# Performance work log

Measured on AMD Instinct MI355X. Metric: run time of the kernel, lower is better.

The kernel has to match this reference:

```python
import jax, jax.numpy as jnp
import numpy as np

B, S, D, H, F = 4, 2048, 1024, 16, 4096
HD = D // H
EPS = 1e-6
ROPE_BASE = 10000.0


def apply_rope(x, positions, head_dim):
    # x: [B, S, H, hd], positions: [B, S]
    fraction = 2.0 * jnp.arange(0, head_dim // 2, dtype=jnp.float32) / head_dim
    timescale = ROPE_BASE ** fraction                      # [hd/2]
    angle = positions[:, :, None, None].astype(jnp.float32) / timescale  # [B,S,1,hd/2]
    sin, cos = jnp.sin(angle), jnp.cos(angle)
    first, second = jnp.split(x, 2, axis=-1)
    return jnp.concatenate([first * cos - second * sin,
                            second * cos + first * sin], axis=-1).astype(x.dtype)


def rms_norm(x, scale):
    var = jnp.mean(jnp.square(x), axis=-1, keepdims=True)
    return (x * jax.lax.rsqrt(var + EPS)) * scale


def setup_inputs() -> dict:
    key = jax.random.key(0)
    ks = jax.random.split(key, 10)
    std = 0.02
    x = jax.random.normal(ks[0], (B, S, D), dtype=jnp.float32)
    segment_positions = jnp.broadcast_to(jnp.arange(S, dtype=jnp.int32), (B, S))
    mask = jnp.broadcast_to(jnp.tril(jnp.ones((S, S), dtype=bool))[None, None], (B, 1, S, S))
    wq = jax.random.normal(ks[1], (D, H, HD), dtype=jnp.float32) * std
    wk = jax.random.normal(ks[2], (D, H, HD), dtype=jnp.float32) * std
    wv = jax.random.normal(ks[3], (D, H, HD), dtype=jnp.float32) * std
    wo = jax.random.normal(ks[4], (H, HD, D), dtype=jnp.float32) * std
    w_gate = jax.random.normal(ks[5], (D, F), dtype=jnp.float32) * std
    w_up = jax.random.normal(ks[6], (D, F), dtype=jnp.float32) * std
    w_down = jax.random.normal(ks[7], (F, D), dtype=jnp.float32) * std
    norm1 = jnp.ones((D,), dtype=jnp.float32)
    norm2 = jnp.ones((D,), dtype=jnp.float32)
    return dict(x=x, segment_positions=segment_positions, mask=mask,
                wq=wq, wk=wk, wv=wv, wo=wo,
                w_gate=w_gate, w_up=w_up, w_down=w_down,
                norm1=norm1, norm2=norm2)


def reference(x, segment_positions, mask, wq, wk, wv, wo, w_gate, w_up, w_down, norm1, norm2):
    # --- pre-norm RoPE attention residual block ---
    h = rms_norm(x, norm1)                                  # [B,S,D]
    q = jnp.einsum('bsd,dhk->bshk', h, wq)                  # [B,S,H,hd]
    k = jnp.einsum('bsd,dhk->bshk', h, wk)
    v = jnp.einsum('bsd,dhk->bshk', h, wv)
    q = apply_rope(q, segment_positions, HD)
    k = apply_rope(k, segment_positions, HD)
    q = q / jnp.sqrt(jnp.float32(HD))
    attn = jnp.einsum('bqhd,bkhd->bhqk', q, k)              # [B,H,S,S]
    big_neg = jnp.finfo(jnp.float32).min
    attn = jnp.where(mask, attn, big_neg)
    attn = jax.nn.softmax(attn, axis=-1)
    ctx = jnp.einsum('bhqk,bkhd->bqhd', attn, v)            # [B,S,H,hd]
    x = x + jnp.einsum('bqhd,hdo->bqo', ctx, wo)            # residual
    # --- pre-norm GLU FFN residual block ---
    h = rms_norm(x, norm2)
    gated = jax.nn.gelu(h @ w_gate) * (h @ w_up)            # [B,S,F]
    x = x + gated @ w_down
    return x
```

## Files before the change

kernel.cpp:

```cpp
#include <hip/hip_runtime.h>
#include <cstdint>
#include <cstddef>

#define BQ 4
#define SQ 2048
#define DQ 1024
#define HQ 16
#define HDQ 64
#define FQ 4096
#define MROWS (BQ * SQ)

typedef __attribute__((ext_vector_type(8))) __bf16 bf16x8;
typedef __attribute__((ext_vector_type(8))) short s16x8;
typedef __attribute__((ext_vector_type(4))) float f32x4;

__device__ __forceinline__ unsigned short f2bf(float f) {
  unsigned int u = __builtin_bit_cast(unsigned int, f);
  u = (u + 0x7FFFu + ((u >> 16) & 1u)) >> 16;
  return (unsigned short)u;
}
__device__ __forceinline__ float bf2f(unsigned short h) {
  unsigned int u = ((unsigned int)h) << 16;
  return __builtin_bit_cast(float, u);
}

typedef const unsigned int __attribute__((address_space(1))) *as1_cu32;
typedef unsigned int __attribute__((address_space(3))) *as3_u32;
#define GLD16(g, l) __builtin_amdgcn_global_load_lds((as1_cu32)(const void*)(g), (as3_u32)(void*)(l), 16, 0, 0)

__global__ __launch_bounds__(256) void k_transpose_bf16(const float* __restrict__ src,
                                                        unsigned short* __restrict__ dst,
                                                        int R, int C) {
  __shared__ float tile[32][33];
  int tx = threadIdx.x & 31, ty = threadIdx.x >> 5;
  int c0 = blockIdx.x * 32, r0 = blockIdx.y * 32;
#pragma unroll
  for (int i = 0; i < 32; i += 8)
    tile[ty + i][tx] = src[(size_t)(r0 + ty + i) * C + (c0 + tx)];
  __syncthreads();
#pragma unroll
  for (int i = 0; i < 32; i += 8)
    dst[(size_t)(c0 + ty + i) * R + (r0 + tx)] = f2bf(tile[tx][ty + i]);
}

__global__ __launch_bounds__(256) void k_rmsnorm(const float* __restrict__ x,
                                                 const float* __restrict__ g,
                                                 unsigned short* __restrict__ out) {
  int row = blockIdx.x, tid = threadIdx.x;
  const float4 v = ((const float4*)(x + (size_t)row * DQ))[tid];
  float ss = v.x * v.x + v.y * v.y + v.z * v.z + v.w * v.w;
#pragma unroll
  for (int d = 32; d >= 1; d >>= 1) ss += __shfl_xor(ss, d);
  __shared__ float ws4[4];
  if ((tid & 63) == 0) ws4[tid >> 6] = ss;
  __syncthreads();
  float tot = ws4[0] + ws4[1] + ws4[2] + ws4[3];
  float r = rsqrtf(tot * (1.0f / DQ) + 1e-6f);
  const float4 gv = ((const float4*)g)[tid];
  ushort4 o;
  o.x = f2bf(v.x * r * gv.x);
  o.y = f2bf(v.y * r * gv.y);
  o.z = f2bf(v.z * r * gv.z);
  o.w = f2bf(v.w * r * gv.w);
  ((ushort4*)(out + (size_t)row * DQ))[tid] = o;
}

template <int MODE>
__global__ __launch_bounds__(256) void k_gemm_bt(const unsigned short* __restrict__ A,
                                                 const unsigned short* __restrict__ Bt,
                                                 void* __restrict__ Cp,
                                                 const float* __restrict__ Res,
                                                 int M, int N, int K) {
  __shared__ __align__(16) unsigned short As[128 * 32];
  __shared__ __align__(16) unsigned short Bs[128 * 32];
  const int tid = threadIdx.x;
  const int lane = tid & 63, w = tid >> 6;
  const int m0 = blockIdx.y * 128, n0 = blockIdx.x * 128;
  const int wm = (w >> 1) * 64, wn = (w & 1) * 64;
  const int lr = lane & 15, lg = lane >> 4;
  f32x4 acc[4][4] = {};
  for (int k0 = 0; k0 < K; k0 += 32) {
#pragma unroll
    for (int i = 0; i < 2; ++i) {
      int flat = i * 256 + tid;
      int row = flat >> 2, ch = flat & 3;
      GLD16(A + (size_t)(m0 + row) * K + k0 + ch * 8, As + (size_t)(i * 256 + w * 64) * 8);
      GLD16(Bt + (size_t)(n0 + row) * K + k0 + ch * 8, Bs + (size_t)(i * 256 + w * 64) * 8);
    }
    __syncthreads();
    bf16x8 af[4], bfr[4];
#pragma unroll
    for (int mi = 0; mi < 4; ++mi)
      af[mi] = *(const bf16x8*)(As + (wm + mi * 16 + lr) * 32 + lg * 8);
#pragma unroll
    for (int ni = 0; ni < 4; ++ni)
      bfr[ni] = *(const bf16x8*)(Bs + (wn + ni * 16 + lr) * 32 + lg * 8);
#pragma unroll
    for (int mi = 0; mi < 4; ++mi)
#pragma unroll
      for (int ni = 0; ni < 4; ++ni)
        acc[mi][ni] = __builtin_amdgcn_mfma_f32_16x16x32_bf16(af[mi], bfr[ni], acc[mi][ni], 0, 0, 0);
    __syncthreads();
  }
#pragma unroll
  for (int mi = 0; mi < 4; ++mi) {
#pragma unroll
    for (int r = 0; r < 4; ++r) {
      int gr = m0 + wm + mi * 16 + lg * 4 + r;
#pragma unroll
      for (int ni = 0; ni < 4; ++ni) {
        int gc = n0 + wn + ni * 16 + lr;
        size_t idx = (size_t)gr * N + gc;
        float v = acc[mi][ni][r];
        if (MODE == 0) {
          ((unsigned short*)Cp)[idx] = f2bf(v);
        } else if (MODE == 1) {
          ((float*)Cp)[idx] = v + Res[idx];
        } else {
          float u = bf2f(((unsigned short*)Cp)[idx]);
          float t = v + 0.044715f * v * v * v;
          float gl = 0.5f * v * (1.0f + tanhf(0.7978845608028654f * t));
          ((unsigned short*)Cp)[idx] = f2bf(gl * u);
        }
      }
    }
  }
}

__global__ __launch_bounds__(512) void k_rope(const unsigned short* __restrict__ qkv,
                                              const int* __restrict__ pos,
                                              unsigned short* __restrict__ qp,
                                              unsigned short* __restrict__ kp,
                                              unsigned short* __restrict__ vp) {
  int bs = blockIdx.x;
  int b = bs >> 11, s = bs & 2047;
  int t = threadIdx.x;
  int hh = t >> 5, j = t & 31;
  float fp = (float)pos[bs];
  const unsigned short* row = qkv + (size_t)bs * 3072;
  float q1 = bf2f(row[hh * 64 + j]);
  float q2 = bf2f(row[hh * 64 + 32 + j]);
  float k1 = bf2f(row[1024 + hh * 64 + j]);
  float k2 = bf2f(row[1024 + hh * 64 + 32 + j]);
  float ts = powf(10000.0f, (float)j * (1.0f / 32.0f));
  float ang = fp / ts;
  float sn = sinf(ang), cs = cosf(ang);
  size_t o = ((size_t)(b * HQ + hh) * SQ + s) * HDQ + j;
  qp[o]      = f2bf((q1 * cs - q2 * sn) * 0.125f);
  qp[o + 32] = f2bf((q2 * cs + q1 * sn) * 0.125f);
  kp[o]      = f2bf(k1 * cs - k2 * sn);
  kp[o + 32] = f2bf(k2 * cs + k1 * sn);
  vp[o]      = row[2048 + hh * 64 + j];
  vp[o + 32] = row[2048 + hh * 64 + 32 + j];
}

__global__ __launch_bounds__(256) void k_flash(const unsigned short* __restrict__ qp,
                                               const unsigned short* __restrict__ kp,
                                               const unsigned short* __restrict__ vp,
                                               unsigned short* __restrict__ ctx) {
  int qb = (int)gridDim.x - 1 - (int)blockIdx.x;
  int bh = blockIdx.y;
  int b = bh >> 4, hh = bh & 15;
  __shared__ __align__(16) unsigned short Ks[32 * 64];
  __shared__ __align__(16) unsigned short Vt[64 * 40];
  __shared__ __align__(16) unsigned short Ps[4][16 * 32];
  int tid = threadIdx.x, lane = tid & 63, w = tid >> 6;
  const int lr = lane & 15, lg = lane >> 4;
  size_t hoff = (size_t)bh * SQ * HDQ;
  const unsigned short* Q = qp + hoff;
  const unsigned short* Kg = kp + hoff;
  const unsigned short* Vg = vp + hoff;
  int qr0 = qb * 64 + w * 16;
  bf16x8 aq0 = *(const bf16x8*)(Q + (size_t)(qr0 + lr) * 64 + lg * 8);
  bf16x8 aq1 = *(const bf16x8*)(Q + (size_t)(qr0 + lr) * 64 + 32 + lg * 8);
  f32x4 accO[4] = {};
  float mrow[4] = {-1e30f, -1e30f, -1e30f, -1e30f};
  float lrow[4] = {0.f, 0.f, 0.f, 0.f};
  int nt = qb * 2 + 2;
  for (int t = 0; t < nt; ++t) {
    int kv0 = t * 32;
    {
      int krow = tid >> 3, ch = tid & 7;
      GLD16(Kg + (size_t)(kv0 + krow) * 64 + ch * 8, Ks + (size_t)(w * 64) * 8);
    }
    {
      int rr = tid & 31, cb = (tid >> 5) * 8;
      bf16x8 vv = *(const bf16x8*)(Vg + (size_t)(kv0 + rr) * 64 + cb);
      s16x8 vs = __builtin_bit_cast(s16x8, vv);
#pragma unroll
      for (int jj = 0; jj < 8; ++jj)
        Vt[(cb + jj) * 40 + rr] = (unsigned short)vs[jj];
    }
    __syncthreads();
    f32x4 sacc[2] = {};
#pragma unroll
    for (int nh = 0; nh < 2; ++nh) {
      bf16x8 bk0 = *(const bf16x8*)(Ks + (nh * 16 + lr) * 64 + lg * 8);
      bf16x8 bk1 = *(const bf16x8*)(Ks + (nh * 16 + lr) * 64 + 32 + lg * 8);
      sacc[nh] = __builtin_amdgcn_mfma_f32_16x16x32_bf16(aq0, bk0, sacc[nh], 0, 0, 0);
      sacc[nh] = __builtin_amdgcn_mfma_f32_16x16x32_bf16(aq1, bk1, sacc[nh], 0, 0, 0);
    }
    float scl[4];
#pragma unroll
    for (int i = 0; i < 4; ++i) {
      int gr = qr0 + lg * 4 + i;
      float s0 = sacc[0][i], s1 = sacc[1][i];
      if (kv0 + lr > gr) s0 = -1e30f;
      if (kv0 + 16 + lr > gr) s1 = -1e30f;
      float mt = fmaxf(s0, s1);
#pragma unroll
      for (int dd = 8; dd >= 1; dd >>= 1) mt = fmaxf(mt, __shfl_xor(mt, dd));
      float mnew = fmaxf(mrow[i], mt);
      scl[i] = __expf(mrow[i] - mnew);
      float p0 = __expf(s0 - mnew), p1 = __expf(s1 - mnew);
      float ps = p0 + p1;
#pragma unroll
      for (int dd = 8; dd >= 1; dd >>= 1) ps += __shfl_xor(ps, dd);
      lrow[i] = lrow[i] * scl[i] + ps;
      mrow[i] = mnew;
      int prow = lg * 4 + i;
      Ps[w][prow * 32 + lr] = f2bf(p0);
      Ps[w][prow * 32 + 16 + lr] = f2bf(p1);
    }
#pragma unroll
    for (int n2 = 0; n2 < 4; ++n2) {
#pragma unroll
      for (int i = 0; i < 4; ++i) accO[n2][i] *= scl[i];
    }
    bf16x8 ap = *(const bf16x8*)(&Ps[w][lr * 32 + lg * 8]);
#pragma unroll
    for (int n2 = 0; n2 < 4; ++n2) {
      bf16x8 bv = *(const bf16x8*)(Vt + (n2 * 16 + lr) * 40 + lg * 8);
      accO[n2] = __builtin_amdgcn_mfma_f32_16x16x32_bf16(ap, bv, accO[n2], 0, 0, 0);
    }
    __syncthreads();
  }
  float linv[4];
#pragma unroll
  for (int i = 0; i < 4; ++i) linv[i] = 1.0f / lrow[i];
#pragma unroll
  for (int n2 = 0; n2 < 4; ++n2) {
#pragma unroll
    for (int i = 0; i < 4; ++i) {
      int gs = qr0 + lg * 4 + i;
      int gc = n2 * 16 + lr;
      ctx[((size_t)b * SQ + gs) * DQ + hh * 64 + gc] = f2bf(accO[n2][i] * linv[i]);
    }
  }
}

extern "C" void kernel_launch(void* const* d_in, const int* in_sizes, int n_in,
                              void* d_out, int out_size, void* d_ws, size_t ws_size,
                              hipStream_t stream) {
  (void)in_sizes; (void)n_in; (void)out_size; (void)ws_size;
  const float* x   = (const float*)d_in[0];
  const int*   pos = (const int*)d_in[1];
  const float* wq  = (const float*)d_in[3];
  const float* wk  = (const float*)d_in[4];
  const float* wv  = (const float*)d_in[5];
  const float* wo  = (const float*)d_in[6];
  const float* wg  = (const float*)d_in[7];
  const float* wu  = (const float*)d_in[8];
  const float* wd  = (const float*)d_in[9];
  const float* n1  = (const float*)d_in[10];
  const float* n2v = (const float*)d_in[11];
  char* ws = (char*)d_ws;
  const size_t MB = 1024ull * 1024ull;
  unsigned short* qkvT  = (unsigned short*)(ws);
  unsigned short* woT   = (unsigned short*)(ws + 6 * MB);
  unsigned short* gateT = (unsigned short*)(ws + 8 * MB);
  unsigned short* upT   = (unsigned short*)(ws + 16 * MB);
  unsigned short* downT = (unsigned short*)(ws + 24 * MB);
  unsigned short* qkv   = (unsigned short*)(ws + 32 * MB);
  unsigned short* act   = qkv;
  unsigned short* qpb   = (unsigned short*)(ws + 80 * MB);
  unsigned short* kpb   = (unsigned short*)(ws + 96 * MB);
  unsigned short* vpb   = (unsigned short*)(ws + 112 * MB);
  unsigned short* hbuf  = (unsigned short*)(ws + 128 * MB);
  unsigned short* ctx   = hbuf;
  float*          x2    = (float*)(ws + 144 * MB);
  unsigned short* h2    = (unsigned short*)(ws + 176 * MB);
  float*          out   = (float*)d_out;

  dim3 b256(256);
  k_transpose_bf16<<<dim3(32, 32), b256, 0, stream>>>(wq, qkvT, 1024, 1024);
  k_transpose_bf16<<<dim3(32, 32), b256, 0, stream>>>(wk, qkvT + 1024 * 1024, 1024, 1024);
  k_transpose_bf16<<<dim3(32, 32), b256, 0, stream>>>(wv, qkvT + 2 * 1024 * 1024, 1024, 1024);
  k_transpose_bf16<<<dim3(32, 32), b256, 0, stream>>>(wo, woT, 1024, 1024);
  k_transpose_bf16<<<dim3(128, 32), b256, 0, stream>>>(wg, gateT, 1024, 4096);
  k_transpose_bf16<<<dim3(128, 32), b256, 0, stream>>>(wu, upT, 1024, 4096);
  k_transpose_bf16<<<dim3(32, 128), b256, 0, stream>>>(wd, downT, 4096, 1024);
  k_rmsnorm<<<MROWS, b256, 0, stream>>>(x, n1, hbuf);
  k_gemm_bt<0><<<dim3(24, 64), b256, 0, stream>>>(hbuf, qkvT, qkv, nullptr, MROWS, 3072, 1024);
  k_rope<<<MROWS, dim3(512), 0, stream>>>(qkv, pos, qpb, kpb, vpb);
  k_flash<<<dim3(32, 64), b256, 0, stream>>>(qpb, kpb, vpb, ctx);
  k_gemm_bt<1><<<dim3(8, 64), b256, 0, stream>>>(ctx, woT, x2, x, MROWS, 1024, 1024);
  k_rmsnorm<<<MROWS, b256, 0, stream>>>(x2, n2v, h2);
  k_gemm_bt<0><<<dim3(32, 64), b256, 0, stream>>>(h2, upT, act, nullptr, MROWS, 4096, 1024);
  k_gemm_bt<2><<<dim3(32, 64), b256, 0, stream>>>(h2, gateT, act, nullptr, MROWS, 4096, 1024);
  k_gemm_bt<1><<<dim3(8, 64), b256, 0, stream>>>(act, downT, out, x2, MROWS, 1024, 4096);
}
```

Measured before the change: 1.002 ms.

## Double-buffer flash attention with 64-wide KV tiles and pre-transposed V

The RoPE kernel now processes 64-row tiles per head with vectorized loads and stores, and writes V pre-transposed through shared memory. It also folds log2(e) into the Q scale so the attention kernel can use exp2. The flash kernel loads 64-key K and V tiles asynchronously into XOR-swizzled, double-buffered LDS, which removes the per-thread V transpose and overlaps the next tile's load with compute. It also masks only on the diagonal tile and defers the row-sum shuffle reduction to the end. The cost is more LDS per block, which may reduce occupancy.

```diff
diff --git a/kernel.cpp b/kernel.cpp
--- a/kernel.cpp
+++ b/kernel.cpp
@@ -11,7 +11,7 @@
 #define MROWS (BQ * SQ)
 
 typedef __attribute__((ext_vector_type(8))) __bf16 bf16x8;
-typedef __attribute__((ext_vector_type(8))) short s16x8;
+typedef __attribute__((ext_vector_type(8))) unsigned short u16x8;
 typedef __attribute__((ext_vector_type(4))) float f32x4;
 
 __device__ __forceinline__ unsigned short f2bf(float f) {
@@ -127,126 +127,177 @@
   }
 }
 
-__global__ __launch_bounds__(512) void k_rope(const unsigned short* __restrict__ qkv,
+__global__ __launch_bounds__(256) void k_rope(const unsigned short* __restrict__ qkv,
                                               const int* __restrict__ pos,
                                               unsigned short* __restrict__ qp,
                                               unsigned short* __restrict__ kp,
-                                              unsigned short* __restrict__ vp) {
-  int bs = blockIdx.x;
-  int b = bs >> 11, s = bs & 2047;
-  int t = threadIdx.x;
-  int hh = t >> 5, j = t & 31;
-  float fp = (float)pos[bs];
-  const unsigned short* row = qkv + (size_t)bs * 3072;
-  float q1 = bf2f(row[hh * 64 + j]);
-  float q2 = bf2f(row[hh * 64 + 32 + j]);
-  float k1 = bf2f(row[1024 + hh * 64 + j]);
-  float k2 = bf2f(row[1024 + hh * 64 + 32 + j]);
-  float ts = powf(10000.0f, (float)j * (1.0f / 32.0f));
-  float ang = fp / ts;
-  float sn = sinf(ang), cs = cosf(ang);
-  size_t o = ((size_t)(b * HQ + hh) * SQ + s) * HDQ + j;
-  qp[o]      = f2bf((q1 * cs - q2 * sn) * 0.125f);
-  qp[o + 32] = f2bf((q2 * cs + q1 * sn) * 0.125f);
-  kp[o]      = f2bf(k1 * cs - k2 * sn);
-  kp[o + 32] = f2bf(k2 * cs + k1 * sn);
-  vp[o]      = row[2048 + hh * 64 + j];
-  vp[o + 32] = row[2048 + hh * 64 + 32 + j];
+                                              unsigned short* __restrict__ vpT) {
+  __shared__ unsigned short T[64 * 67];
+  const float NEG_L2TS = -0.4152410118609203f;
+  const float QSCALE = 0.125f * 1.4426950408889634f;
+  int bh = blockIdx.y, b = bh >> 4, hh = bh & 15;
+  int s0 = blockIdx.x * 64;
+  int tid = threadIdx.x;
+  int row = tid >> 2, q4 = tid & 3, j0 = q4 * 8;
+  int gs = s0 + row;
+  const unsigned short* base = qkv + ((size_t)(b * SQ + gs)) * 3072 + hh * 64;
+  u16x8 q1 = *(const u16x8*)(base + j0);
+  u16x8 q2 = *(const u16x8*)(base + 32 + j0);
+  u16x8 k1 = *(const u16x8*)(base + 1024 + j0);
+  u16x8 k2 = *(const u16x8*)(base + 1024 + 32 + j0);
+  u16x8 v1 = *(const u16x8*)(base + 2048 + j0);
+  u16x8 v2 = *(const u16x8*)(base + 2048 + 32 + j0);
+  float fp = (float)pos[b * SQ + gs];
+  u16x8 oq1, oq2, ok1, ok2;
+#pragma unroll
+  for (int jj = 0; jj < 8; ++jj) {
+    float ang = fp * exp2f((float)(j0 + jj) * NEG_L2TS);
+    float sn, cs;
+    __sincosf(ang, &sn, &cs);
+    float q1f = bf2f(q1[jj]), q2f = bf2f(q2[jj]);
+    float k1f = bf2f(k1[jj]), k2f = bf2f(k2[jj]);
+    oq1[jj] = f2bf((q1f * cs - q2f * sn) * QSCALE);
+    oq2[jj] = f2bf((q2f * cs + q1f * sn) * QSCALE);
+    ok1[jj] = f2bf(k1f * cs - k2f * sn);
+    ok2[jj] = f2bf(k2f * cs + k1f * sn);
+    T[row * 67 + j0 + jj] = v1[jj];
+    T[row * 67 + 32 + j0 + jj] = v2[jj];
+  }
+  size_t o = ((size_t)bh * SQ + gs) * 64;
+  *(u16x8*)(qp + o + j0) = oq1;
+  *(u16x8*)(qp + o + 32 + j0) = oq2;
+  *(u16x8*)(kp + o + j0) = ok1;
+  *(u16x8*)(kp + o + 32 + j0) = ok2;
+  __syncthreads();
+  int hd = tid >> 2;
+#pragma unroll
+  for (int c2 = 0; c2 < 2; ++c2) {
+    int sb = q4 * 16 + c2 * 8;
+    u16x8 ov;
+#pragma unroll
+    for (int ii = 0; ii < 8; ++ii) ov[ii] = T[(sb + ii) * 67 + hd];
+    *(u16x8*)(vpT + ((size_t)bh * 64 + hd) * SQ + s0 + sb) = ov;
+  }
 }
 
 __global__ __launch_bounds__(256) void k_flash(const unsigned short* __restrict__ qp,
                                                const unsigned short* __restrict__ kp,
-                                               const unsigned short* __restrict__ vp,
+                                               const unsigned short* __restrict__ vpT,
                                                unsigned short* __restrict__ ctx) {
-  int qb = (int)gridDim.x - 1 - (int)blockIdx.x;
-  int bh = blockIdx.y;
-  int b = bh >> 4, hh = bh & 15;
-  __shared__ __align__(16) unsigned short Ks[32 * 64];
-  __shared__ __align__(16) unsigned short Vt[64 * 40];
-  __shared__ __align__(16) unsigned short Ps[4][16 * 32];
+  __shared__ __align__(16) unsigned short Ks[2][64 * 64];
+  __shared__ __align__(16) unsigned short Vs[2][64 * 64];
+  __shared__ __align__(16) unsigned short Ps[4][16 * 64];
+  int qb = 31 - (int)blockIdx.x;
+  int bh = blockIdx.y, b = bh >> 4, hh = bh & 15;
   int tid = threadIdx.x, lane = tid & 63, w = tid >> 6;
   const int lr = lane & 15, lg = lane >> 4;
-  size_t hoff = (size_t)bh * SQ * HDQ;
+  const int key = lr & 7;
+  size_t hoff = (size_t)bh * SQ * 64;
   const unsigned short* Q = qp + hoff;
   const unsigned short* Kg = kp + hoff;
-  const unsigned short* Vg = vp + hoff;
+  const unsigned short* Vh = vpT + hoff;
   int qr0 = qb * 64 + w * 16;
   bf16x8 aq0 = *(const bf16x8*)(Q + (size_t)(qr0 + lr) * 64 + lg * 8);
   bf16x8 aq1 = *(const bf16x8*)(Q + (size_t)(qr0 + lr) * 64 + 32 + lg * 8);
   f32x4 accO[4] = {};
   float mrow[4] = {-1e30f, -1e30f, -1e30f, -1e30f};
   float lrow[4] = {0.f, 0.f, 0.f, 0.f};
-  int nt = qb * 2 + 2;
+  int nt = qb + 1;
+
+#define STAGE(d, t)                                                              \
+  {                                                                              \
+    int kv0s = (t) * 64;                                                         \
+    _Pragma("unroll") for (int i = 0; i < 2; ++i) {                              \
+      int flat = i * 256 + tid;                                                  \
+      int srow = flat >> 3;                                                      \
+      int ch = (flat & 7) ^ (srow & 7);                                          \
+      GLD16(Kg + (size_t)(kv0s + srow) * 64 + ch * 8, &Ks[d][(i * 256 + w * 64) * 8]); \
+      GLD16(Vh + (size_t)srow * SQ + kv0s + ch * 8, &Vs[d][(i * 256 + w * 64) * 8]);   \
+    }                                                                            \
+  }
+
+  STAGE(0, 0);
+  __syncthreads();
   for (int t = 0; t < nt; ++t) {
-    int kv0 = t * 32;
-    {
-      int krow = tid >> 3, ch = tid & 7;
-      GLD16(Kg + (size_t)(kv0 + krow) * 64 + ch * 8, Ks + (size_t)(w * 64) * 8);
-    }
-    {
-      int rr = tid & 31, cb = (tid >> 5) * 8;
-      bf16x8 vv = *(const bf16x8*)(Vg + (size_t)(kv0 + rr) * 64 + cb);
-      s16x8 vs = __builtin_bit_cast(s16x8, vv);
-#pragma unroll
-      for (int jj = 0; jj < 8; ++jj)
-        Vt[(cb + jj) * 40 + rr] = (unsigned short)vs[jj];
+    int kv0 = t * 64;
+    if (t + 1 < nt) STAGE((t + 1) & 1, t + 1);
+    const unsigned short* Kc = Ks[t & 1];
+    const unsigned short* Vc = Vs[t & 1];
+    f32x4 sacc[4] = {};
+#pragma unroll
+    for (int nh = 0; nh < 4; ++nh) {
+      const unsigned short* kr = Kc + (nh * 16 + lr) * 64;
+      bf16x8 b0 = *(const bf16x8*)(kr + (lg ^ key) * 8);
+      bf16x8 b1 = *(const bf16x8*)(kr + ((lg + 4) ^ key) * 8);
+      sacc[nh] = __builtin_amdgcn_mfma_f32_16x16x32_bf16(aq0, b0, sacc[nh], 0, 0, 0);
+      sacc[nh] = __builtin_amdgcn_mfma_f32_16x16x32_bf16(aq1, b1, sacc[nh], 0, 0, 0);
+    }
+    bool diag = (t == qb);
+    float scl[4];
+#pragma unroll
+    for (int i = 0; i < 4; ++i) {
+      float s0 = sacc[0][i], s1 = sacc[1][i], s2 = sacc[2][i], s3 = sacc[3][i];
+      if (diag) {
+        int gr = qr0 + lg * 4 + i;
+        int c = kv0 + lr;
+        if (c > gr) s0 = -1e30f;
+        if (c + 16 > gr) s1 = -1e30f;
+        if (c + 32 > gr) s2 = -1e30f;
+        if (c + 48 > gr) s3 = -1e30f;
+      }
+      float mt = fmaxf(fmaxf(s0, s1), fmaxf(s2, s3));
+      mt = fmaxf(mt, __shfl_xor(mt, 1));
+      mt = fmaxf(mt, __shfl_xor(mt, 2));
+      mt = fmaxf(mt, __shfl_xor(mt, 4));
+      mt = fmaxf(mt, __shfl_xor(mt, 8));
+      float mnew = fmaxf(mrow[i], mt);
+      scl[i] = exp2f(mrow[i] - mnew);
+      mrow[i] = mnew;
+      float p0 = exp2f(s0 - mnew), p1 = exp2f(s1 - mnew);
+      float p2 = exp2f(s2 - mnew), p3 = exp2f(s3 - mnew);
+      lrow[i] = lrow[i] * scl[i] + (p0 + p1 + p2 + p3);
+      int prow = lg * 4 + i;
+      unsigned short* Pr = &Ps[w][prow * 64];
+      int pk = prow & 7;
+      int sub = lr >> 3, off = lr & 7;
+      Pr[((0 + sub) ^ pk) * 8 + off] = f2bf(p0);
+      Pr[((2 + sub) ^ pk) * 8 + off] = f2bf(p1);
+      Pr[((4 + sub) ^ pk) * 8 + off] = f2bf(p2);
+      Pr[((6 + sub) ^ pk) * 8 + off] = f2bf(p3);
+    }
+#pragma unroll
+    for (int n2 = 0; n2 < 4; ++n2)
+#pragma unroll
+      for (int i = 0; i < 4; ++i) accO[n2][i] *= scl[i];
+    bf16x8 ap0 = *(const bf16x8*)(&Ps[w][lr * 64] + (lg ^ key) * 8);
+    bf16x8 ap1 = *(const bf16x8*)(&Ps[w][lr * 64] + ((lg + 4) ^ key) * 8);
+#pragma unroll
+    for (int n2 = 0; n2 < 4; ++n2) {
+      const unsigned short* vr = Vc + (n2 * 16 + lr) * 64;
+      bf16x8 bv0 = *(const bf16x8*)(vr + (lg ^ key) * 8);
+      bf16x8 bv1 = *(const bf16x8*)(vr + ((lg + 4) ^ key) * 8);
+      accO[n2] = __builtin_amdgcn_mfma_f32_16x16x32_bf16(ap0, bv0, accO[n2], 0, 0, 0);
+      accO[n2] = __builtin_amdgcn_mfma_f32_16x16x32_bf16(ap1, bv1, accO[n2], 0, 0, 0);
     }
     __syncthreads();
-    f32x4 sacc[2] = {};
-#pragma unroll
-    for (int nh = 0; nh < 2; ++nh) {
-      bf16x8 bk0 = *(const bf16x8*)(Ks + (nh * 16 + lr) * 64 + lg * 8);
-      bf16x8 bk1 = *(const bf16x8*)(Ks + (nh * 16 + lr) * 64 + 32 + lg * 8);
-      sacc[nh] = __builtin_amdgcn_mfma_f32_16x16x32_bf16(aq0, bk0, sacc[nh], 0, 0, 0);
-      sacc[nh] = __builtin_amdgcn_mfma_f32_16x16x32_bf16(aq1, bk1, sacc[nh], 0, 0, 0);
-    }
-    float scl[4];
-#pragma unroll
-    for (int i = 0; i < 4; ++i) {
-      int gr = qr0 + lg * 4 + i;
-      float s0 = sacc[0][i], s1 = sacc[1][i];
-      if (kv0 + lr > gr) s0 = -1e30f;
-      if (kv0 + 16 + lr > gr) s1 = -1e30f;
-      float mt = fmaxf(s0, s1);
-#pragma unroll
-      for (int dd = 8; dd >= 1; dd >>= 1) mt = fmaxf(mt, __shfl_xor(mt, dd));
-      float mnew = fmaxf(mrow[i], mt);
-      scl[i] = __expf(mrow[i] - mnew);
-      float p0 = __expf(s0 - mnew), p1 = __expf(s1 - mnew);
-      float ps = p0 + p1;
-#pragma unroll
-      for (int dd = 8; dd >= 1; dd >>= 1) ps += __shfl_xor(ps, dd);
-      lrow[i] = lrow[i] * scl[i] + ps;
-      mrow[i] = mnew;
-      int prow = lg * 4 + i;
-      Ps[w][prow * 32 + lr] = f2bf(p0);
-      Ps[w][prow * 32 + 16 + lr] = f2bf(p1);
-    }
-#pragma unroll
-    for (int n2 = 0; n2 < 4; ++n2) {
-#pragma unroll
-      for (int i = 0; i < 4; ++i) accO[n2][i] *= scl[i];
-    }
-    bf16x8 ap = *(const bf16x8*)(&Ps[w][lr * 32 + lg * 8]);
-#pragma unroll
-    for (int n2 = 0; n2 < 4; ++n2) {
-      bf16x8 bv = *(const bf16x8*)(Vt + (n2 * 16 + lr) * 40 + lg * 8);
-      accO[n2] = __builtin_amdgcn_mfma_f32_16x16x32_bf16(ap, bv, accO[n2], 0, 0, 0);
-    }
-    __syncthreads();
-  }
-  float linv[4];
-#pragma unroll
-  for (int i = 0; i < 4; ++i) linv[i] = 1.0f / lrow[i];
-#pragma unroll
-  for (int n2 = 0; n2 < 4; ++n2) {
+  }
+#pragma unroll
+  for (int i = 0; i < 4; ++i) {
+    float l = lrow[i];
+    l += __shfl_xor(l, 1);
+    l += __shfl_xor(l, 2);
+    l += __shfl_xor(l, 4);
+    l += __shfl_xor(l, 8);
+    lrow[i] = 1.0f / l;
+  }
+#pragma unroll
+  for (int n2 = 0; n2 < 4; ++n2)
 #pragma unroll
     for (int i = 0; i < 4; ++i) {
       int gs = qr0 + lg * 4 + i;
-      int gc = n2 * 16 + lr;
-      ctx[((size_t)b * SQ + gs) * DQ + hh * 64 + gc] = f2bf(accO[n2][i] * linv[i]);
-    }
-  }
+      ctx[((size_t)b * SQ + gs) * DQ + hh * 64 + n2 * 16 + lr] = f2bf(accO[n2][i] * lrow[i]);
+    }
+#undef STAGE
 }
 
 extern "C" void kernel_launch(void* const* d_in, const int* in_sizes, int n_in,
@@ -275,7 +326,7 @@
   unsigned short* act   = qkv;
   unsigned short* qpb   = (unsigned short*)(ws + 80 * MB);
   unsigned short* kpb   = (unsigned short*)(ws + 96 * MB);
-  unsigned short* vpb   = (unsigned short*)(ws + 112 * MB);
+  unsigned short* vpT   = (unsigned short*)(ws + 112 * MB);
   unsigned short* hbuf  = (unsigned short*)(ws + 128 * MB);
   unsigned short* ctx   = hbuf;
   float*          x2    = (float*)(ws + 144 * MB);
@@ -292,8 +343,8 @@
   k_transpose_bf16<<<dim3(32, 128), b256, 0, stream>>>(wd, downT, 4096, 1024);
   k_rmsnorm<<<MROWS, b256, 0, stream>>>(x, n1, hbuf);
   k_gemm_bt<0><<<dim3(24, 64), b256, 0, stream>>>(hbuf, qkvT, qkv, nullptr, MROWS, 3072, 1024);
-  k_rope<<<MROWS, dim3(512), 0, stream>>>(qkv, pos, qpb, kpb, vpb);
-  k_flash<<<dim3(32, 64), b256, 0, stream>>>(qpb, kpb, vpb, ctx);
+  k_rope<<<dim3(32, 64), b256, 0, stream>>>(qkv, pos, qpb, kpb, vpT);
+  k_flash<<<dim3(32, 64), b256, 0, stream>>>(qpb, kpb, vpT, ctx);
   k_gemm_bt<1><<<dim3(8, 64), b256, 0, stream>>>(ctx, woT, x2, x, MROWS, 1024, 1024);
   k_rmsnorm<<<MROWS, b256, 0, stream>>>(x2, n2v, h2);
   k_gemm_bt<0><<<dim3(32, 64), b256, 0, stream>>>(h2, upT, act, nullptr, MROWS, 4096, 1024);
```

Result: faster. 840.5 us (-16.1%).
